# Kernel tuning notes

Hardware: AMD Instinct MI355X
Metric: run time of the kernel (lower is better)

## Reference

```python
import jax, jax.numpy as jnp
import numpy as np

B, G, C = 16384, 7, 30  # batch, 7x7 grid, 2*5 box params + 20 classes


def setup_inputs() -> dict:
    key = jax.random.key(0)
    k1, k2 = jax.random.split(key)
    pred = jax.random.uniform(k1, (B, G, G, C), dtype=jnp.float32)
    labels = jax.random.uniform(k2, (B, G, G, C), dtype=jnp.float32)
    # channel 0 of labels is the object-presence indicator (==1 where a gt box exists)
    labels = labels.at[..., 0].set((labels[..., 0] > 0.7).astype(jnp.float32))
    return {"pred": pred, "labels": labels}


def _corners(box):
    # box channels: [conf, x, y, w, h]
    x, y, w, h = box[..., 1], box[..., 2], box[..., 3], box[..., 4]
    return x - 0.5 * w, x + 0.5 * w, y - 0.5 * h, y + 0.5 * h  # left,right,top,bottom


def _iou(b1, b2):
    l1, r1, t1, bt1 = _corners(b1)
    l2, r2, t2, bt2 = _corners(b2)
    in_h = jnp.minimum(bt1, bt2) - jnp.maximum(t1, t2)
    in_w = jnp.minimum(r1, r2) - jnp.maximum(l1, l2)
    inter = jnp.where((in_h < 0) | (in_w < 0), 0.0, in_h * in_w)
    area1 = (bt1 - t1) * (r1 - l1)
    area2 = (bt2 - t2) * (r2 - l2)
    return inter / (area1 + area2 - inter)


def reference(pred, labels):
    mask = labels[..., 0]                     # [B,7,7] object indicator (0/1)
    box1 = pred[..., 0:5]
    box2 = pred[..., 5:10]
    gt = labels[..., 0:5]
    iou1 = _iou(box1, gt)
    iou2 = _iou(box2, gt)
    best = iou1 >= iou2                       # responsible box per cell
    sel = jnp.where(best[..., None], box1, box2)
    iou_max = jnp.where(best, iou1, iou2)
    iou_min = jnp.where(best, iou2, iou1)
    center = 5.0 * ((sel[..., 1] - gt[..., 1]) ** 2 + (sel[..., 2] - gt[..., 2]) ** 2)
    wh = 5.0 * ((jnp.sqrt(sel[..., 3]) - jnp.sqrt(gt[..., 3])) ** 2
                + (jnp.sqrt(sel[..., 4]) - jnp.sqrt(gt[..., 4])) ** 2)
    cls = jnp.sum((pred[..., 10:] - labels[..., 10:]) ** 2, axis=-1)

    def msum(x):
        return jnp.sum(x * mask)

    # [center, wh, obj_conf, noobj_conf, classification]
    return jnp.stack([msum(center), msum(wh), msum(iou_max), msum(iou_min), msum(cls)])
```

## Files before the change

### kernel.cpp

```cpp
#include <hip/hip_runtime.h>
#include <stdint.h>

#define NCH   30
#define TPB   256
#define TILE  64
#define TW    (TILE * NCH)
#define TF4   (TW / 4)
#define NBLK  1536

__device__ __forceinline__ float iou_f(float x1, float y1, float w1, float h1,
                                       float x2, float y2, float w2, float h2) {
    float l1 = x1 - 0.5f * w1, r1 = x1 + 0.5f * w1;
    float t1 = y1 - 0.5f * h1, b1 = y1 + 0.5f * h1;
    float l2 = x2 - 0.5f * w2, r2 = x2 + 0.5f * w2;
    float t2 = y2 - 0.5f * h2, b2 = y2 + 0.5f * h2;
    float in_h = fminf(b1, b2) - fmaxf(t1, t2);
    float in_w = fminf(r1, r2) - fmaxf(l1, l2);
    float inter = (in_h < 0.f || in_w < 0.f) ? 0.f : in_h * in_w;
    float a1 = (b1 - t1) * (r1 - l1);
    float a2 = (b2 - t2) * (r2 - l2);
    return inter / (a1 + a2 - inter);
}

__device__ __forceinline__ void cell_loss(const float* __restrict__ pp,
                                          const float* __restrict__ lp,
                                          float& v0, float& v1, float& v2,
                                          float& v3, float& v4) {
    const float2 l01 = *(const float2*)(lp);
    const float mask = l01.x;
    if (mask == 0.f) return;

    const float2 l23 = *(const float2*)(lp + 2);
    const float2 l45 = *(const float2*)(lp + 4);
    const float gx = l01.y, gy = l23.x, gw = l23.y, gh = l45.x;

    const float2 p01 = *(const float2*)(pp);
    const float2 p23 = *(const float2*)(pp + 2);
    const float2 p45 = *(const float2*)(pp + 4);
    const float2 p67 = *(const float2*)(pp + 6);
    const float2 p89 = *(const float2*)(pp + 8);

    const float i1 = iou_f(p01.y, p23.x, p23.y, p45.x, gx, gy, gw, gh);
    const float i2 = iou_f(p67.x, p67.y, p89.x, p89.y, gx, gy, gw, gh);
    const bool best = (i1 >= i2);
    const float sx = best ? p01.y : p67.x;
    const float sy = best ? p23.x : p67.y;
    const float sw = best ? p23.y : p89.x;
    const float sh = best ? p45.x : p89.y;
    const float imax = best ? i1 : i2;
    const float imin = best ? i2 : i1;

    const float center = 5.f * ((sx - gx) * (sx - gx) + (sy - gy) * (sy - gy));
    const float dw = sqrtf(sw) - sqrtf(gw);
    const float dh = sqrtf(sh) - sqrtf(gh);
    const float wh = 5.f * (dw * dw + dh * dh);

    float cls = 0.f;
#pragma unroll
    for (int k = 0; k < 10; ++k) {
        const float2 pd = *(const float2*)(pp + 10 + 2 * k);
        const float2 ld = *(const float2*)(lp + 10 + 2 * k);
        const float dx = pd.x - ld.x;
        const float dy = pd.y - ld.y;
        cls += dx * dx + dy * dy;
    }

    v0 += center * mask;
    v1 += wh * mask;
    v2 += imax * mask;
    v3 += imin * mask;
    v4 += cls * mask;
}

__global__ __launch_bounds__(TPB) void yolo_partial(const float* __restrict__ pred,
                                                    const float* __restrict__ lab,
                                                    float* __restrict__ partial,
                                                    int n_cells) {
    __shared__ float sp[TW];
    __shared__ float sl[2][TW];
    __shared__ unsigned long long sbits;
    __shared__ float red[5][TPB / 64];

    const int tid  = threadIdx.x;
    const int wave = tid >> 6;
    const int lane = tid & 63;
    const int bid  = blockIdx.x;
    const int NB   = gridDim.x;
    const int nt   = n_cells / TILE;

    const int  idx0 = tid;
    const int  idx1 = TPB + tid;
    const bool has1 = (idx1 < TF4);

    const int c00 = (4 * idx0) / NCH, c01 = (4 * idx0 + 3) / NCH;
    const int c10 = has1 ? (4 * idx1) / NCH : 0;
    const int c11 = has1 ? (4 * idx1 + 3) / NCH : 0;

    float v0 = 0.f, v1 = 0.f, v2 = 0.f, v3 = 0.f, v4 = 0.f;

    int cur = 0;
    unsigned long long bits = 0;

    if (bid < nt) {
        {
            const size_t gbase = (size_t)bid * TW;
            float4 l0 = *(const float4*)(lab + gbase + (size_t)idx0 * 4);
            float4 l1;
            if (has1) l1 = *(const float4*)(lab + gbase + (size_t)idx1 * 4);
            *(float4*)(&sl[0][idx0 * 4]) = l0;
            if (has1) *(float4*)(&sl[0][idx1 * 4]) = l1;
        }
        __syncthreads();
        {
            const unsigned long long b =
                __ballot(tid < TILE && sl[0][tid * NCH] != 0.f);
            if (tid == 0) sbits = b;
        }
        __syncthreads();
        bits = sbits;

        for (int t = bid; t < nt; t += NB) {
            const int  nxt = cur ^ 1;
            const bool have_next = (t + NB < nt);
            const size_t gbase = (size_t)t * TW;

            float4 p0, p1, l0, l1;
            const bool need0 = (((bits >> c00) & 1ull) | ((bits >> c01) & 1ull));
            const bool need1 = has1 &&
                               (((bits >> c10) & 1ull) | ((bits >> c11) & 1ull));
            if (need0) p0 = *(const float4*)(pred + gbase + (size_t)idx0 * 4);
            if (need1) p1 = *(const float4*)(pred + gbase + (size_t)idx1 * 4);
            if (have_next) {
                const size_t nbase = (size_t)(t + NB) * TW;
                l0 = *(const float4*)(lab + nbase + (size_t)idx0 * 4);
                if (has1) l1 = *(const float4*)(lab + nbase + (size_t)idx1 * 4);
            }

            if (need0) *(float4*)(&sp[idx0 * 4]) = p0;
            if (need1) *(float4*)(&sp[idx1 * 4]) = p1;
            if (have_next) {
                *(float4*)(&sl[nxt][idx0 * 4]) = l0;
                if (has1) *(float4*)(&sl[nxt][idx1 * 4]) = l1;
            }
            __syncthreads();

            if (tid < TILE)
                cell_loss(sp + tid * NCH, &sl[cur][tid * NCH],
                          v0, v1, v2, v3, v4);

            unsigned long long b = 0;
            if (have_next)
                b = __ballot(tid < TILE && sl[nxt][tid * NCH] != 0.f);
            if (tid == 0) sbits = b;
            __syncthreads();
            bits = sbits;
            cur = nxt;
        }
    }

    const int rem_start = nt * TILE;
    if (bid == 0 && rem_start < n_cells) {
        for (int c = rem_start + tid; c < n_cells; c += TPB) {
            cell_loss(pred + (size_t)c * NCH, lab + (size_t)c * NCH,
                      v0, v1, v2, v3, v4);
        }
    }

#pragma unroll
    for (int off = 32; off > 0; off >>= 1) {
        v0 += __shfl_down(v0, off);
        v1 += __shfl_down(v1, off);
        v2 += __shfl_down(v2, off);
        v3 += __shfl_down(v3, off);
        v4 += __shfl_down(v4, off);
    }
    if (lane == 0) {
        red[0][wave] = v0;
        red[1][wave] = v1;
        red[2][wave] = v2;
        red[3][wave] = v3;
        red[4][wave] = v4;
    }
    __syncthreads();
    if (tid < 5) {
        float sacc = 0.f;
#pragma unroll
        for (int w = 0; w < TPB / 64; ++w) sacc += red[tid][w];
        partial[(size_t)bid * 5 + tid] = sacc;
    }
}

__global__ __launch_bounds__(256) void final_reduce(const float* __restrict__ partial,
                                                    float* __restrict__ out,
                                                    int n_blocks) {
    __shared__ float red[5][4];
    const int tid = threadIdx.x;
    float v0 = 0.f, v1 = 0.f, v2 = 0.f, v3 = 0.f, v4 = 0.f;
    for (int b = tid; b < n_blocks; b += 256) {
        const float* p = partial + (size_t)b * 5;
        v0 += p[0]; v1 += p[1]; v2 += p[2]; v3 += p[3]; v4 += p[4];
    }
#pragma unroll
    for (int off = 32; off > 0; off >>= 1) {
        v0 += __shfl_down(v0, off);
        v1 += __shfl_down(v1, off);
        v2 += __shfl_down(v2, off);
        v3 += __shfl_down(v3, off);
        v4 += __shfl_down(v4, off);
    }
    const int wave = tid >> 6;
    const int lane = tid & 63;
    if (lane == 0) {
        red[0][wave] = v0;
        red[1][wave] = v1;
        red[2][wave] = v2;
        red[3][wave] = v3;
        red[4][wave] = v4;
    }
    __syncthreads();
    if (tid < 5) {
        float sacc = 0.f;
#pragma unroll
        for (int w = 0; w < 4; ++w) sacc += red[tid][w];
        out[tid] = sacc;
    }
}

extern "C" void kernel_launch(void* const* d_in, const int* in_sizes, int n_in,
                              void* d_out, int out_size, void* d_ws, size_t ws_size,
                              hipStream_t stream) {
    const float* pred = (const float*)d_in[0];
    const float* lab  = (const float*)d_in[1];
    float* out = (float*)d_out;
    float* partial = (float*)d_ws;

    const int n_cells = in_sizes[0] / NCH;

    hipLaunchKernelGGL(yolo_partial, dim3(NBLK), dim3(TPB), 0, stream,
                       pred, lab, partial, n_cells);
    hipLaunchKernelGGL(final_reduce, dim3(1), dim3(256), 0, stream,
                       partial, out, NBLK);
}
```

Measured before the change: 201.3 us.

## Prefetch mask bits two tiles ahead to skip loading unused label chunks

The kernel now reads only the object-presence flag of each cell two tiles ahead and ballots it into a bitmask. The next tile's label data is then loaded only for float4 chunks overlapping occupied cells, as was already done for predictions. The mask multiply is dropped inside the tile loop because the bitmask already gates the computation. This cuts label bandwidth by about 70% for sparse masks, at the cost of an extra scattered scalar load per tile and a longer dependency chain of bitmasks.

```diff
diff --git a/kernel.cpp b/kernel.cpp
--- a/kernel.cpp
+++ b/kernel.cpp
@@ -22,14 +22,11 @@
     return inter / (a1 + a2 - inter);
 }
 
-__device__ __forceinline__ void cell_loss(const float* __restrict__ pp,
-                                          const float* __restrict__ lp,
-                                          float& v0, float& v1, float& v2,
-                                          float& v3, float& v4) {
+__device__ __forceinline__ void cell_loss_nm(const float* __restrict__ pp,
+                                             const float* __restrict__ lp,
+                                             float& v0, float& v1, float& v2,
+                                             float& v3, float& v4) {
     const float2 l01 = *(const float2*)(lp);
-    const float mask = l01.x;
-    if (mask == 0.f) return;
-
     const float2 l23 = *(const float2*)(lp + 2);
     const float2 l45 = *(const float2*)(lp + 4);
     const float gx = l01.y, gy = l23.x, gw = l23.y, gh = l45.x;
@@ -65,11 +62,22 @@
         cls += dx * dx + dy * dy;
     }
 
-    v0 += center * mask;
-    v1 += wh * mask;
-    v2 += imax * mask;
-    v3 += imin * mask;
-    v4 += cls * mask;
+    v0 += center;
+    v1 += wh;
+    v2 += imax;
+    v3 += imin;
+    v4 += cls;
+}
+
+__device__ __forceinline__ void cell_loss(const float* __restrict__ pp,
+                                          const float* __restrict__ lp,
+                                          float& v0, float& v1, float& v2,
+                                          float& v3, float& v4) {
+    const float mask = lp[0];
+    if (mask == 0.f) return;
+    float a = 0.f, b = 0.f, c = 0.f, d = 0.f, e = 0.f;
+    cell_loss_nm(pp, lp, a, b, c, d, e);
+    v0 += a * mask; v1 += b * mask; v2 += c * mask; v3 += d * mask; v4 += e * mask;
 }
 
 __global__ __launch_bounds__(TPB) void yolo_partial(const float* __restrict__ pred,
@@ -78,7 +86,7 @@
                                                     int n_cells) {
     __shared__ float sp[TW];
     __shared__ float sl[2][TW];
-    __shared__ unsigned long long sbits;
+    __shared__ unsigned long long sbits[2];
     __shared__ float red[5][TPB / 64];
 
     const int tid  = threadIdx.x;
@@ -99,61 +107,71 @@
     float v0 = 0.f, v1 = 0.f, v2 = 0.f, v3 = 0.f, v4 = 0.f;
 
     int cur = 0;
-    unsigned long long bits = 0;
+    unsigned long long bits_cur = 0, bits_next = 0;
 
     if (bid < nt) {
         {
+            const float m0 = (tid < TILE)
+                ? lab[(size_t)bid * TW + (size_t)tid * NCH] : 0.f;
+            const float m1 = (tid < TILE && bid + NB < nt)
+                ? lab[(size_t)(bid + NB) * TW + (size_t)tid * NCH] : 0.f;
+            const unsigned long long b0 = __ballot(m0 != 0.f);
+            const unsigned long long b1 = __ballot(m1 != 0.f);
+            if (tid == 0) { sbits[0] = b0; sbits[1] = b1; }
+        }
+        __syncthreads();
+        bits_cur  = sbits[0];
+        bits_next = sbits[1];
+
+        {
             const size_t gbase = (size_t)bid * TW;
-            float4 l0 = *(const float4*)(lab + gbase + (size_t)idx0 * 4);
-            float4 l1;
-            if (has1) l1 = *(const float4*)(lab + gbase + (size_t)idx1 * 4);
-            *(float4*)(&sl[0][idx0 * 4]) = l0;
-            if (has1) *(float4*)(&sl[0][idx1 * 4]) = l1;
-        }
-        __syncthreads();
-        {
-            const unsigned long long b =
-                __ballot(tid < TILE && sl[0][tid * NCH] != 0.f);
-            if (tid == 0) sbits = b;
-        }
-        __syncthreads();
-        bits = sbits;
+            const bool n0 = (((bits_cur >> c00) | (bits_cur >> c01)) & 1ull);
+            const bool n1 = has1 && (((bits_cur >> c10) | (bits_cur >> c11)) & 1ull);
+            if (n0) *(float4*)(&sl[0][idx0 * 4]) =
+                        *(const float4*)(lab + gbase + (size_t)idx0 * 4);
+            if (n1) *(float4*)(&sl[0][idx1 * 4]) =
+                        *(const float4*)(lab + gbase + (size_t)idx1 * 4);
+        }
 
         for (int t = bid; t < nt; t += NB) {
-            const int  nxt = cur ^ 1;
-            const bool have_next = (t + NB < nt);
+            const int  nxt   = cur ^ 1;
+            const bool have1 = (t + NB < nt);
+            const bool have2 = (t + 2 * NB < nt);
             const size_t gbase = (size_t)t * TW;
 
             float4 p0, p1, l0, l1;
-            const bool need0 = (((bits >> c00) & 1ull) | ((bits >> c01) & 1ull));
-            const bool need1 = has1 &&
-                               (((bits >> c10) & 1ull) | ((bits >> c11) & 1ull));
-            if (need0) p0 = *(const float4*)(pred + gbase + (size_t)idx0 * 4);
-            if (need1) p1 = *(const float4*)(pred + gbase + (size_t)idx1 * 4);
-            if (have_next) {
+            const bool pn0 = (((bits_cur >> c00) | (bits_cur >> c01)) & 1ull);
+            const bool pn1 = has1 && (((bits_cur >> c10) | (bits_cur >> c11)) & 1ull);
+            if (pn0) p0 = *(const float4*)(pred + gbase + (size_t)idx0 * 4);
+            if (pn1) p1 = *(const float4*)(pred + gbase + (size_t)idx1 * 4);
+
+            bool ln0 = false, ln1 = false;
+            if (have1) {
                 const size_t nbase = (size_t)(t + NB) * TW;
-                l0 = *(const float4*)(lab + nbase + (size_t)idx0 * 4);
-                if (has1) l1 = *(const float4*)(lab + nbase + (size_t)idx1 * 4);
+                ln0 = (((bits_next >> c00) | (bits_next >> c01)) & 1ull);
+                ln1 = has1 && (((bits_next >> c10) | (bits_next >> c11)) & 1ull);
+                if (ln0) l0 = *(const float4*)(lab + nbase + (size_t)idx0 * 4);
+                if (ln1) l1 = *(const float4*)(lab + nbase + (size_t)idx1 * 4);
             }
 
-            if (need0) *(float4*)(&sp[idx0 * 4]) = p0;
-            if (need1) *(float4*)(&sp[idx1 * 4]) = p1;
-            if (have_next) {
-                *(float4*)(&sl[nxt][idx0 * 4]) = l0;
-                if (has1) *(float4*)(&sl[nxt][idx1 * 4]) = l1;
-            }
+            const float md = (tid < TILE && have2)
+                ? lab[(size_t)(t + 2 * NB) * TW + (size_t)tid * NCH] : 0.f;
+
+            if (pn0) *(float4*)(&sp[idx0 * 4]) = p0;
+            if (pn1) *(float4*)(&sp[idx1 * 4]) = p1;
+            if (ln0) *(float4*)(&sl[nxt][idx0 * 4]) = l0;
+            if (ln1) *(float4*)(&sl[nxt][idx1 * 4]) = l1;
             __syncthreads();
 
-            if (tid < TILE)
-                cell_loss(sp + tid * NCH, &sl[cur][tid * NCH],
-                          v0, v1, v2, v3, v4);
-
-            unsigned long long b = 0;
-            if (have_next)
-                b = __ballot(tid < TILE && sl[nxt][tid * NCH] != 0.f);
-            if (tid == 0) sbits = b;
+            if (tid < TILE && ((bits_cur >> tid) & 1ull))
+                cell_loss_nm(sp + tid * NCH, &sl[cur][tid * NCH],
+                             v0, v1, v2, v3, v4);
+
+            const unsigned long long bd = __ballot(md != 0.f);
+            if (tid == 0) sbits[0] = bd;
             __syncthreads();
-            bits = sbits;
+            bits_cur  = bits_next;
+            bits_next = sbits[0];
             cur = nxt;
         }
     }
```

Measured after the change: 207.7 us. +3.2%, slower.
